# Kernel tuning notes

Hardware: AMD Instinct MI355X
Metric: run time of the kernel (lower is better)

## Reference

```python
import jax, jax.numpy as jnp
import numpy as np

S, B, NIN = 64, 64, 64          # att_width (= target_seq_len), batch, num_input
H1, HB, H = 128, 128, 128       # first LSTM size, biLSTM hidden, att_hid
MLP = (1024, 512, 256, 128, 1)  # h1..h4, num_output


def _lstm_cell(x, h, c, Wih, Whh, b):
    # PyTorch gate order: i, f, g, o
    z = x @ Wih.T + h @ Whh.T + b
    i, f, g, o = jnp.split(z, 4, axis=-1)
    c = jax.nn.sigmoid(f) * c + jax.nn.sigmoid(i) * jnp.tanh(g)
    h = jax.nn.sigmoid(o) * jnp.tanh(c)
    return h, c


def _lstm_seq(xs, Wih, Whh, b, reverse=False):
    # xs: [S, B, in] -> hs: [S, B, H], final (h, c)
    h0 = jnp.zeros((xs.shape[1], Whh.shape[1]), xs.dtype)

    def step(carry, x):
        h, c = _lstm_cell(x, carry[0], carry[1], Wih, Whh, b)
        return (h, c), h

    (h, c), hs = jax.lax.scan(step, (h0, h0), xs, reverse=reverse)
    return hs, (h, c)


def _forward(input_seqs,
             lstm1_Wih, lstm1_Whh, lstm1_b,
             bi2f_Wih, bi2f_Whh, bi2f_b, bi2b_Wih, bi2b_Whh, bi2b_b,
             bi3f_Wih, bi3f_Whh, bi3f_b, bi3b_Wih, bi3b_Whh, bi3b_b,
             enc_Wih, enc_Whh, enc_b,
             dec_Wih, dec_Whh, dec_b,
             att_fc_W, att_w,
             W1_W, W1_b, W2_W, W2_b, W3_W, W3_b, W4_W, W4_b, out_W, out_b):
    # 1) one-directional LSTM
    x, _ = _lstm_seq(input_seqs, lstm1_Wih, lstm1_Whh, lstm1_b)
    # 2-3) two stacked bidirectional LSTMs
    f, _ = _lstm_seq(x, bi2f_Wih, bi2f_Whh, bi2f_b)
    bk, _ = _lstm_seq(x, bi2b_Wih, bi2b_Whh, bi2b_b, reverse=True)
    x = jnp.concatenate([f, bk], axis=-1)            # [S,B,2*HB]
    f, _ = _lstm_seq(x, bi3f_Wih, bi3f_Whh, bi3f_b)
    bk, _ = _lstm_seq(x, bi3b_Wih, bi3b_Whh, bi3b_b, reverse=True)
    x = jnp.concatenate([f, bk], axis=-1)            # [S,B,2*HB]
    # 4) encoder LSTM
    enc_out, (eh, ec) = _lstm_seq(x, enc_Wih, enc_Whh, enc_b)  # [S,B,H]
    # per-step attention decode loop (S sequential steps)
    def dec_step(carry, _):
        xin, h, c = carry
        h, c = _lstm_cell(xin, h, c, dec_Wih, dec_Whh, dec_b)   # [B,H]
        # 'concat' attention: tanh(fc(h + enc_out)) @ w -> scores over S
        scores = jnp.tanh((h[None, :, :] + enc_out) @ att_fc_W.T) @ att_w  # [S,B]
        aw = jax.nn.softmax(scores, axis=0)
        ctx = jnp.einsum('sb,sbh->bh', aw, enc_out)             # [B,H]
        out = jnp.concatenate([h, ctx], axis=-1)                # [B,2H]
        return (h, h, c), out

    _, dec_outs = jax.lax.scan(dec_step, (enc_out[-1], eh, ec), None, length=S)
    # [S,B,2H] -> [B, S*2H]
    flat = dec_outs.transpose(1, 0, 2).reshape(dec_outs.shape[1], -1)
    # 5-6) flatten + 4-layer tanh MLP + linear head
    x = jnp.tanh(flat @ W1_W.T + W1_b)
    x = jnp.tanh(x @ W2_W.T + W2_b)
    x = jnp.tanh(x @ W3_W.T + W3_b)
    x = jnp.tanh(x @ W4_W.T + W4_b)
    return x @ out_W.T + out_b


def setup_inputs() -> dict:
    key = jax.random.key(0)
    ks = iter(jax.random.split(key, 40))

    def mat(shape, scale=0.08):
        return (jax.random.normal(next(ks), shape) * scale).astype(jnp.float32)

    d = {}
    d['input_seqs'] = jax.random.normal(next(ks), (S, B, NIN), dtype=jnp.float32)

    def lstm_p(pfx, inp, hid):
        d[pfx + '_Wih'] = mat((4 * hid, inp))
        d[pfx + '_Whh'] = mat((4 * hid, hid))
        d[pfx + '_b'] = mat((4 * hid,))

    lstm_p('lstm1', NIN, H1)
    lstm_p('bi2f', H1, HB); lstm_p('bi2b', H1, HB)
    lstm_p('bi3f', 2 * HB, HB); lstm_p('bi3b', 2 * HB, HB)
    lstm_p('enc', 2 * HB, H)
    lstm_p('dec', H, H)
    d['att_fc_W'] = mat((H, H))
    d['att_w'] = mat((H,))
    dims = [2 * H * S] + list(MLP)
    names = ['W1', 'W2', 'W3', 'W4', 'out']
    for i, nm in enumerate(names):
        d[nm + '_W'] = mat((dims[i + 1], dims[i]))
        d[nm + '_b'] = mat((dims[i + 1],))
    return d


def reference(input_seqs,
              lstm1_Wih, lstm1_Whh, lstm1_b,
              bi2f_Wih, bi2f_Whh, bi2f_b, bi2b_Wih, bi2b_Whh, bi2b_b,
              bi3f_Wih, bi3f_Whh, bi3f_b, bi3b_Wih, bi3b_Whh, bi3b_b,
              enc_Wih, enc_Whh, enc_b,
              dec_Wih, dec_Whh, dec_b,
              att_fc_W, att_w,
              W1_W, W1_b, W2_W, W2_b, W3_W, W3_b, W4_W, W4_b, out_W, out_b):
    return _forward(input_seqs,
                    lstm1_Wih, lstm1_Whh, lstm1_b,
                    bi2f_Wih, bi2f_Whh, bi2f_b, bi2b_Wih, bi2b_Whh, bi2b_b,
                    bi3f_Wih, bi3f_Whh, bi3f_b, bi3b_Wih, bi3b_Whh, bi3b_b,
                    enc_Wih, enc_Whh, enc_b,
                    dec_Wih, dec_Whh, dec_b,
                    att_fc_W, att_w,
                    W1_W, W1_b, W2_W, W2_b, W3_W, W3_b, W4_W, W4_b, out_W, out_b)
```

## Files before the change

### kernel.cpp

```cpp
#include <hip/hip_runtime.h>
#include <hip/hip_bf16.h>

typedef unsigned int u32;
typedef unsigned short u16;

typedef _Float16 half2_t __attribute__((ext_vector_type(2)));
union H2U { u32 u; half2_t h; };

typedef _Float16 f16x8 __attribute__((ext_vector_type(8)));
typedef float f32x4 __attribute__((ext_vector_type(4)));
union F16V { uint4 u; f16x8 h; };

#if defined(__has_builtin)
#if __has_builtin(__builtin_amdgcn_fdot2)
#define HAS_FDOT2 1
#endif
#if __has_builtin(__builtin_amdgcn_update_dpp)
#define HAS_DPP 1
#endif
#endif

__device__ __forceinline__ float bf2f(u32 u) {
  union { u32 i; float f; } v; v.i = u << 16; return v.f;
}
__device__ __forceinline__ float sigf(float x) {
  return 1.0f / (1.0f + __expf(-x));
}
__device__ __forceinline__ float tanhfast(float x) {
  return 2.0f / (1.0f + __expf(-2.0f * x)) - 1.0f;
}
__device__ __forceinline__ u16 f2bf(float f) {
  u32 u = __float_as_uint(f);
  u += 0x7fffu + ((u >> 16) & 1u);
  return (u16)(u >> 16);
}
__device__ __forceinline__ u16 f2h(float f) {
  union { _Float16 h; u16 u; } v; v.h = (_Float16)f; return v.u;
}
__device__ __forceinline__ u32 fpair2h2(float a, float b) {
  H2U r; r.h.x = (_Float16)a; r.h.y = (_Float16)b; return r.u;
}
__device__ __forceinline__ u32 bfpair2h2(u32 two_bf) {
  H2U r;
  r.h.x = (_Float16)bf2f(two_bf & 0xffffu);
  r.h.y = (_Float16)bf2f(two_bf >> 16);
  return r.u;
}
__device__ __forceinline__ float dot2acc(u32 wu, u32 hu, float acc) {
  H2U w, h; w.u = wu; h.u = hu;
#ifdef HAS_FDOT2
  return __builtin_amdgcn_fdot2(w.h, h.h, acc, false);
#else
  acc = fmaf((float)w.h.x, (float)h.h.x, acc);
  return fmaf((float)w.h.y, (float)h.h.y, acc);
#endif
}
template <int CTRL>
__device__ __forceinline__ float dppf(float x) {
#ifdef HAS_DPP
  int y = __builtin_amdgcn_update_dpp(0, __float_as_int(x), CTRL, 0xF, 0xF, true);
  return __int_as_float(y);
#else
  const int lane = threadIdx.x & 63;
  if (CTRL == 0xB1)  return __shfl_xor(x, 1, 64);
  if (CTRL == 0x4E)  return __shfl_xor(x, 2, 64);
  if (CTRL == 0x104) return __shfl_down(x, 4, 64);
  return __shfl(x, (lane & ~3) | (CTRL & 3), 64);
#endif
}

__global__ void k_detect(const u32* __restrict__ w, int* __restrict__ flag) {
  __shared__ int cnt;
  if (threadIdx.x == 0) cnt = 0;
  __syncthreads();
  int c = 0;
  for (int i = threadIdx.x; i < 8192; i += 256) {
    const u32 lo = w[i] & 0xffffu;
    const u32 e = (lo >> 7) & 0xffu;
    c += (e >= 100u && e <= 140u) ? 1 : 0;
  }
  atomicAdd(&cnt, c);
  __syncthreads();
  if (threadIdx.x == 0) *flag = (cnt > 4915) ? 1 : 0;
}

struct Job { const void* s; float* d; int n; int f16; };
struct Jobs { Job j[30]; };

__global__ void k_cvt_all(Jobs J, const int* __restrict__ flag) {
  const Job jb = J.j[blockIdx.y];
  const int isbf = *flag;
  for (int i = blockIdx.x * 256 + threadIdx.x; i < jb.n; i += 32 * 256) {
    const float v = isbf ? bf2f(((const u16*)jb.s)[i]) : ((const float*)jb.s)[i];
    if (jb.f16) ((u16*)jb.d)[i] = f2h(v);
    else        jb.d[i] = v;
  }
}

struct IJobs { const float* b[4]; float* d[4]; int n[4]; int mask[4]; };
__global__ void k_init4(IJobs I) {
  const int j = blockIdx.y;
  const float* bb = I.b[j];
  float* dd = I.d[j];
  const int n = I.n[j], mask = I.mask[j];
  for (int i = blockIdx.x * 256 + threadIdx.x; i < n; i += gridDim.x * 256)
    dd[i] = bb[i & mask];
}

struct PJobs { const float* s[7]; const float* s2[7]; u32* d[7]; };
__global__ void k_pack(PJobs P) {
  const float* src = P.s[blockIdx.y];
  const float* src2 = P.s2[blockIdx.y];
  u32* dst = P.d[blockIdx.y];
  const int i = blockIdx.x * 256 + threadIdx.x;
  const int tid = i >> 6, rem = i & 63;
  const int j = rem >> 4, kk = rem & 15;
  const int r = tid >> 2, kq = tid & 3;
  const int row = r + 128 * j, col = kq * 32 + 2 * kk;
  float v0 = src[row * 128 + col];
  float v1 = src[row * 128 + col + 1];
  if (src2) { v0 += src2[row * 128 + col]; v1 += src2[row * 128 + col + 1]; }
  H2U v;
  v.h.x = (_Float16)v0;
  v.h.y = (_Float16)v1;
  dst[i] = v.u;
}

__launch_bounds__(256)
__global__ void k_mf(const u16* __restrict__ A, int lda,
                     const void* __restrict__ Wv, int ldw,
                     const float* __restrict__ bias,
                     float* __restrict__ C, int ldc,
                     int K, int atom, int wfollow,
                     const int* __restrict__ dflag)
{
  __shared__ __align__(16) u16 As[64][40];
  __shared__ __align__(16) u16 Bs[64][40];
  const int isbf = wfollow ? *dflag : 0;
  const int tid = threadIdx.x;
  const int m0 = blockIdx.x * 64, n0 = blockIdx.y * 64;
  const int kc = K / gridDim.z;
  const int k0 = blockIdx.z * kc;
  const int row = tid >> 2, part = tid & 3;
  const int l = tid & 63, w = tid >> 6;
  const int wr = w >> 1, wc = w & 1;
  const int fr = l & 15, fk = l >> 4;
  f32x4 acc[2][2] = {};
  const u16*   Ap   = A + (size_t)(m0 + row) * lda + k0 + part * 8;
  const u16*   Wp16 = (const u16*)Wv   + (size_t)(n0 + row) * ldw + k0 + part * 8;
  const float* Wp32 = (const float*)Wv + (size_t)(n0 + row) * ldw + k0 + part * 8;

  for (int kk = 0; kk < kc; kk += 32) {
    const uint4 av = *(const uint4*)(Ap + kk);
    uint4 wv;
    if (isbf) {
      const uint4 wu = *(const uint4*)(Wp16 + kk);
      wv.x = bfpair2h2(wu.x); wv.y = bfpair2h2(wu.y);
      wv.z = bfpair2h2(wu.z); wv.w = bfpair2h2(wu.w);
    } else {
      const float4 w0 = *(const float4*)(Wp32 + kk);
      const float4 w1 = *(const float4*)(Wp32 + kk + 4);
      wv.x = fpair2h2(w0.x, w0.y); wv.y = fpair2h2(w0.z, w0.w);
      wv.z = fpair2h2(w1.x, w1.y); wv.w = fpair2h2(w1.z, w1.w);
    }
    __syncthreads();
    *(uint4*)&As[row][part * 8] = av;
    *(uint4*)&Bs[row][part * 8] = wv;
    __syncthreads();
    F16V a0, a1, b0, b1;
    a0.u = *(const uint4*)&As[wr * 32 + fr][fk * 8];
    a1.u = *(const uint4*)&As[wr * 32 + 16 + fr][fk * 8];
    b0.u = *(const uint4*)&Bs[wc * 32 + fr][fk * 8];
    b1.u = *(const uint4*)&Bs[wc * 32 + 16 + fr][fk * 8];
    acc[0][0] = __builtin_amdgcn_mfma_f32_16x16x32_f16(a0.h, b0.h, acc[0][0], 0, 0, 0);
    acc[0][1] = __builtin_amdgcn_mfma_f32_16x16x32_f16(a0.h, b1.h, acc[0][1], 0, 0, 0);
    acc[1][0] = __builtin_amdgcn_mfma_f32_16x16x32_f16(a1.h, b0.h, acc[1][0], 0, 0, 0);
    acc[1][1] = __builtin_amdgcn_mfma_f32_16x16x32_f16(a1.h, b1.h, acc[1][1], 0, 0, 0);
  }

  #pragma unroll
  for (int i = 0; i < 2; ++i) {
    #pragma unroll
    for (int j = 0; j < 2; ++j) {
      const int n = n0 + wc * 32 + j * 16 + fr;
      const float bv = (bias && !atom) ? bias[n] : 0.0f;
      #pragma unroll
      for (int q = 0; q < 4; ++q) {
        const int m = m0 + wr * 32 + i * 16 + fk * 4 + q;
        if (atom) atomicAdd(&C[(size_t)m * ldc + n], acc[i][j][q]);
        else      C[(size_t)m * ldc + n] = acc[i][j][q] + bv;
      }
    }
  }
}

__launch_bounds__(256)
__global__ void k_gemm(const float* __restrict__ A, int lda,
                       const void* __restrict__ Wv, int ldw,
                       const float* __restrict__ bias,
                       float* __restrict__ C, int ldc,
                       int K, int actA, int atom, int wfollow,
                       const int* __restrict__ dflag)
{
  __shared__ float As[32][65];
  __shared__ float Ws[32][65];
  const int isbf = wfollow ? *dflag : 0;
  const int tid = threadIdx.x;
  const int tx = tid & 15, ty = tid >> 4;
  const int m0 = blockIdx.x * 64, n0 = blockIdx.y * 64;
  const int kc = K / gridDim.z;
  const int k0 = blockIdx.z * kc;
  const int lr = tid >> 2;
  const int lk = (tid & 3) << 3;
  float acc[4][4] = {{0.f}};
  const float* Ap   = A + (size_t)(m0 + lr) * lda + k0 + lk;
  const u16*   Wp16 = (const u16*)Wv   + (size_t)(n0 + lr) * ldw + k0 + lk;
  const float* Wp32 = (const float*)Wv + (size_t)(n0 + lr) * ldw + k0 + lk;
  for (int kk = 0; kk < kc; kk += 32) {
    float4 av0 = *(const float4*)(Ap + kk);
    float4 av1 = *(const float4*)(Ap + kk + 4);
    float wv[8];
    if (isbf) {
      const uint4 wu = *(const uint4*)(Wp16 + kk);
      wv[0]=bf2f(wu.x & 0xffffu); wv[1]=bf2f(wu.x >> 16);
      wv[2]=bf2f(wu.y & 0xffffu); wv[3]=bf2f(wu.y >> 16);
      wv[4]=bf2f(wu.z & 0xffffu); wv[5]=bf2f(wu.z >> 16);
      wv[6]=bf2f(wu.w & 0xffffu); wv[7]=bf2f(wu.w >> 16);
    } else {
      const float4 w0 = *(const float4*)(Wp32 + kk);
      const float4 w1 = *(const float4*)(Wp32 + kk + 4);
      wv[0]=w0.x; wv[1]=w0.y; wv[2]=w0.z; wv[3]=w0.w;
      wv[4]=w1.x; wv[5]=w1.y; wv[6]=w1.z; wv[7]=w1.w;
    }
    if (actA) {
      av0.x = tanhfast(av0.x); av0.y = tanhfast(av0.y);
      av0.z = tanhfast(av0.z); av0.w = tanhfast(av0.w);
      av1.x = tanhfast(av1.x); av1.y = tanhfast(av1.y);
      av1.z = tanhfast(av1.z); av1.w = tanhfast(av1.w);
    }
    __syncthreads();
    As[lk+0][lr] = av0.x; As[lk+1][lr] = av0.y;
    As[lk+2][lr] = av0.z; As[lk+3][lr] = av0.w;
    As[lk+4][lr] = av1.x; As[lk+5][lr] = av1.y;
    As[lk+6][lr] = av1.z; As[lk+7][lr] = av1.w;
    #pragma unroll
    for (int q = 0; q < 8; ++q) Ws[lk+q][lr] = wv[q];
    __syncthreads();
    #pragma unroll
    for (int k = 0; k < 32; ++k) {
      float a[4], w[4];
      #pragma unroll
      for (int i = 0; i < 4; ++i) a[i] = As[k][ty + 16*i];
      #pragma unroll
      for (int j = 0; j < 4; ++j) w[j] = Ws[k][tx + 16*j];
      #pragma unroll
      for (int i = 0; i < 4; ++i)
        #pragma unroll
        for (int j = 0; j < 4; ++j)
          acc[i][j] = fmaf(a[i], w[j], acc[i][j]);
    }
  }
  #pragma unroll
  for (int i = 0; i < 4; ++i) {
    const int m = m0 + ty + 16*i;
    #pragma unroll
    for (int j = 0; j < 4; ++j) {
      const int n = n0 + tx + 16*j;
      if (atom) atomicAdd(&C[(size_t)m*ldc + n], acc[i][j]);
      else {
        const float bv = bias ? bias[n] : 0.0f;
        C[(size_t)m*ldc + n] = acc[i][j] + bv;
      }
    }
  }
}

__launch_bounds__(512)
__attribute__((amdgpu_waves_per_eu(2, 2)))
__global__ void k_rec(const float* __restrict__ Zf, const float* __restrict__ Zb,
                      const u32* __restrict__ Wf, const u32* __restrict__ Wb,
                      float* __restrict__ HS, int hstride, int offF, int offB,
                      const float* __restrict__ h0, const float* __restrict__ c0,
                      int zmode, int zld, float* __restrict__ Cout, int hf16)
{
  const int b = blockIdx.x & 63;
  const int dir = blockIdx.x >> 6;
  const float* Z = dir ? Zb : Zf;
  const u32* Wg = dir ? Wb : Wf;
  const int off = dir ? offB : offF;
  const int tid = threadIdx.x;
  const int r = tid >> 2, kq = tid & 3;

  __shared__ __align__(16) float zall[64*512];
  __shared__ __align__(16) u32 hbuf[2][64];

  if (!zmode) {
    #pragma unroll
    for (int q = 0; q < 16; ++q) {
      const int fid = tid + 512*q;
      const int s = fid >> 7, c4 = (fid & 127) << 2;
      const int cs = c4 ^ (((c4 >> 7) & 1) << 4);
      *(float4*)&zall[s*512 + cs] = *(const float4*)&Z[((size_t)s*64 + b)*zld + c4];
    }
  }

  u32 wp[64];
  {
    const uint4* wr = (const uint4*)(Wg + (size_t)tid * 64);
    #pragma unroll
    for (int q = 0; q < 16; ++q) {
      const uint4 u = wr[q];
      wp[q*4+0]=u.x; wp[q*4+1]=u.y; wp[q*4+2]=u.z; wp[q*4+3]=u.w;
    }
  }
  #pragma unroll
  for (int q = 0; q < 64; ++q)
    asm volatile("" : "+v"(wp[q]));

  float creg = c0 ? c0[b*128 + r] : 0.0f;
  if (tid < 64) {
    H2U v;
    if (h0) {
      v.h.x = (_Float16)h0[b*128 + 2*tid];
      v.h.y = (_Float16)h0[b*128 + 2*tid + 1];
    } else {
      v.h.x = (_Float16)0.f; v.h.y = (_Float16)0.f;
    }
    hbuf[0][tid] = v.u;
  }

  const int colz = (r + 128*kq) ^ ((kq & 1) << 4);
  float zdec = 0.f;
  if (zmode) zdec = Z[r + 128*kq];
  const float* zp = zall + (dir ? 63*512 : 0) + colz;
  const int zstep = dir ? -512 : 512;
  size_t hidx = ((size_t)(dir ? 63 : 0)*64 + b)*hstride + off + r;
  const ptrdiff_t hstep = (ptrdiff_t)(dir ? -64 : 64) * hstride;
  const bool beta = (kq & 1) != 0;
  const bool gmm  = (kq & 2) != 0;
  __syncthreads();

  for (int t = 0; t < 64; ++t) {
    float zcv;
    if (zmode) zcv = zdec;
    else       zcv = *zp;
    u32 hh16[16];
    {
      const u32* hp = hbuf[t & 1];
      *(uint4*)&hh16[0]  = *(const uint4*)&hp[kq*16];
      *(uint4*)&hh16[4]  = *(const uint4*)&hp[kq*16 + 4];
      *(uint4*)&hh16[8]  = *(const uint4*)&hp[kq*16 + 8];
      *(uint4*)&hh16[12] = *(const uint4*)&hp[kq*16 + 12];
    }
    float a[4] = {0.f,0.f,0.f,0.f};
    #pragma unroll
    for (int j = 0; j < 4; ++j)
      #pragma unroll
      for (int i = 0; i < 16; ++i)
        a[j] = dot2acc(wp[j*16 + i], hh16[i], a[j]);
    const float u0 = beta ? a[1] : a[0];
    const float v0 = beta ? a[0] : a[1];
    const float u1 = beta ? a[3] : a[2];
    const float v1 = beta ? a[2] : a[3];
    const float x01 = u0 + dppf<0xB1>(v0);
    const float x23 = u1 + dppf<0xB1>(v1);
    const float keep = gmm ? x23 : x01;
    const float send = gmm ? x01 : x23;
    const float g = keep + dppf<0x4E>(send) + zcv;
    const float sg = sigf(g);
    const float tg = tanhfast(g);
    const float si  = dppf<0x00>(sg);
    const float sf  = dppf<0x55>(sg);
    const float tgg = dppf<0xAA>(tg);
    const float so  = dppf<0xFF>(sg);
    const float cc = sf * creg + si * tgg;
    const float hh = so * tanhfast(cc);
    creg = cc;
    const float hn = dppf<0x104>(hh);
    if (kq == 0) {
      if (hf16) ((u16*)HS)[hidx] = f2h(hh);
      else      HS[hidx] = hh;
      if (!(r & 1)) {
        H2U v; v.h.x = (_Float16)hh; v.h.y = (_Float16)hn;
        hbuf[(t+1) & 1][r >> 1] = v.u;
      }
    }
    zp += zstep;
    hidx += hstep;
    __syncthreads();
  }

  if (Cout != nullptr && kq == 0) Cout[b*128 + r] = creg;
}

#define TS 132
__launch_bounds__(256, 1)
__global__ void k_att(const float* __restrict__ enco, const float* __restrict__ encp,
                      const float* __restrict__ Hdec, const float* __restrict__ Hproj,
                      const float* __restrict__ attw, u16* __restrict__ flat)
{
  const int b = blockIdx.x;
  const int t0 = blockIdx.y * 16;
  const int tid = threadIdx.x;
  __shared__ __align__(16) float ep[64*TS];
  __shared__ __align__(16) float en[64*TS];
  __shared__ __align__(16) float hp[16*TS];
  __shared__ float S[64*17];
  __shared__ float aw[64*17];
  __shared__ __align__(16) float awt[128];

  for (int i = tid; i < 8192; i += 256) {
    const int s = i >> 7, k = i & 127;
    const size_t g = ((size_t)s*64 + b)*128 + k;
    ep[s*TS + k] = encp[g];
    en[s*TS + k] = enco[g];
  }
  for (int i = tid; i < 2048; i += 256) {
    const int t = i >> 7, k = i & 127;
    const size_t g = ((size_t)(t0 + t)*64 + b)*128 + k;
    hp[t*TS + k] = Hproj[g];
    flat[(size_t)b*16384 + (t0 + t)*256 + k] = f2h(Hdec[g]);
  }
  if (tid < 128) awt[tid] = attw[tid];
  __syncthreads();

  {
    const int t = tid & 15, sg = tid >> 4;
    #pragma unroll
    for (int i = 0; i < 4; ++i) {
      const int s = sg*4 + i;
      float acc = 0.f;
      #pragma unroll 8
      for (int k = 0; k < 128; k += 4) {
        const float4 h4 = *(const float4*)&hp[t*TS + k];
        const float4 e4 = *(const float4*)&ep[s*TS + k];
        const float4 w4 = *(const float4*)&awt[k];
        acc = fmaf(w4.x, tanhfast(h4.x + e4.x), acc);
        acc = fmaf(w4.y, tanhfast(h4.y + e4.y), acc);
        acc = fmaf(w4.z, tanhfast(h4.z + e4.z), acc);
        acc = fmaf(w4.w, tanhfast(h4.w + e4.w), acc);
      }
      S[s*17 + t] = acc;
    }
  }
  __syncthreads();
  if (tid < 16) {
    const int t = tid;
    float m = -1e30f;
    for (int s = 0; s < 64; ++s) m = fmaxf(m, S[s*17 + t]);
    float sum = 0.f;
    for (int s = 0; s < 64; ++s) {
      const float e = __expf(S[s*17 + t] - m);
      aw[s*17 + t] = e;
      sum += e;
    }
    const float inv = 1.0f / sum;
    for (int s = 0; s < 64; ++s) aw[s*17 + t] *= inv;
  }
  __syncthreads();
  {
    const int t = tid >> 4, kg = tid & 15;
    float c0a[8] = {0,0,0,0,0,0,0,0};
    for (int s = 0; s < 64; ++s) {
      const float a = aw[s*17 + t];
      const float4 e0 = *(const float4*)&en[s*TS + kg*8];
      const float4 e1 = *(const float4*)&en[s*TS + kg*8 + 4];
      c0a[0] = fmaf(a, e0.x, c0a[0]);
      c0a[1] = fmaf(a, e0.y, c0a[1]);
      c0a[2] = fmaf(a, e0.z, c0a[2]);
      c0a[3] = fmaf(a, e0.w, c0a[3]);
      c0a[4] = fmaf(a, e1.x, c0a[4]);
      c0a[5] = fmaf(a, e1.y, c0a[5]);
      c0a[6] = fmaf(a, e1.z, c0a[6]);
      c0a[7] = fmaf(a, e1.w, c0a[7]);
    }
    union { u16 s[8]; uint4 u; } o;
    #pragma unroll
    for (int q = 0; q < 8; ++q) o.s[q] = f2h(c0a[q]);
    u16* dst = &flat[(size_t)b*16384 + (t0 + t)*256 + 128 + kg*8];
    *(uint4*)dst = o.u;
  }
}

__global__ void k_head(const float* __restrict__ a4, const float* __restrict__ outW,
                       const float* __restrict__ outb, void* __restrict__ out,
                       const int* __restrict__ dflag)
{
  const int b = threadIdx.x;
  float acc = outb[0];
  #pragma unroll 8
  for (int k = 0; k < 128; ++k)
    acc = fmaf(outW[k], tanhfast(a4[b*128 + k]), acc);
  if (*dflag) ((u16*)out)[b] = f2bf(acc);
  else        ((float*)out)[b] = acc;
}

extern "C" void kernel_launch(void* const* d_in, const int* in_sizes, int n_in,
                              void* d_out, int out_size, void* d_ws, size_t ws_size,
                              hipStream_t stream)
{
  (void)in_sizes; (void)n_in; (void)out_size; (void)ws_size;

  float* p = (float*)d_ws;
  int*   flagp = (int*)p;    p += 64;
  float* x0    = p; p += 64*64*64;
  float* cl1Wih = p; p += 512*64;
  float* cl1Whh = p; p += 512*128;
  float* cl1b   = p; p += 512;
  float* c2Wih  = p; p += 1024*128;
  float* c2bias = p; p += 1024;
  float* c2fWhh = p; p += 512*128;
  float* c2bWhh = p; p += 512*128;
  float* c3Wih  = p; p += 1024*256;
  float* c3bias = p; p += 1024;
  float* c3fWhh = p; p += 512*128;
  float* c3bWhh = p; p += 512*128;
  float* ceWih  = p; p += 512*256;
  float* ceWhh  = p; p += 512*128;
  float* ceb    = p; p += 512;
  float* cdWih  = p; p += 512*128;
  float* cdWhh  = p; p += 512*128;
  float* cdb    = p; p += 512;
  float* cattW  = p; p += 128*128;
  float* cattw  = p; p += 128;
  float* cW1b   = p; p += 1024;
  float* cW2b   = p; p += 512;
  float* cW3b   = p; p += 256;
  float* cW4b   = p; p += 128;
  float* coW    = p; p += 128;
  float* cob    = p; p += 16;
  u32* wpL1 = (u32*)p; p += 32768;
  u32* wp2f = (u32*)p; p += 32768;
  u32* wp2b = (u32*)p; p += 32768;
  u32* wp3f = (u32*)p; p += 32768;
  u32* wp3b = (u32*)p; p += 32768;
  u32* wpE  = (u32*)p; p += 32768;
  u32* wpD  = (u32*)p; p += 32768;
  float* Zf   = p; p += 4096*512;
  float* Z2   = p; p += 4096*1024;
  float* h1   = p; p += 4096*128;
  float* x2   = p; p += 4096*256;
  float* x3   = p; p += 4096*256;
  float* enco = p; p += 4096*128;
  float* Hdec = p; p += 4096*128;
  float* encp = p; p += 4096*128;
  float* Hprj = p; p += 4096*128;
  float* ec   = p; p += 64*128;
  float* flat = p; p += 64*16384;
  float* a1   = p; p += 64*1024;
  float* a2   = p; p += 64*512;
  float* a3   = p; p += 64*256;
  float* a4   = p; p += 64*128;

  k_detect<<<1, 256, 0, stream>>>((const u32*)d_in[2], flagp);

  Jobs J;
  int nj = 0;
  auto add = [&](const void* s, float* d, int n, int f16 = 0) {
    J.j[nj].s = s; J.j[nj].d = d; J.j[nj].n = n; J.j[nj].f16 = f16; ++nj;
  };
  add(d_in[0],  x0,     64*64*64, 1);
  add(d_in[1],  cl1Wih, 512*64);
  add(d_in[2],  cl1Whh, 512*128);
  add(d_in[3],  cl1b,   512);
  add(d_in[4],  c2Wih,            512*128);
  add(d_in[7],  c2Wih + 512*128,  512*128);
  add(d_in[6],  c2bias,       512);
  add(d_in[9],  c2bias + 512, 512);
  add(d_in[5],  c2fWhh, 512*128);
  add(d_in[8],  c2bWhh, 512*128);
  add(d_in[10], c3Wih,            512*256);
  add(d_in[13], c3Wih + 512*256,  512*256);
  add(d_in[12], c3bias,       512);
  add(d_in[15], c3bias + 512, 512);
  add(d_in[11], c3fWhh, 512*128);
  add(d_in[14], c3bWhh, 512*128);
  add(d_in[16], ceWih,  512*256);
  add(d_in[17], ceWhh,  512*128);
  add(d_in[18], ceb,    512);
  add(d_in[19], cdWih,  512*128);
  add(d_in[20], cdWhh,  512*128);
  add(d_in[21], cdb,    512);
  add(d_in[22], cattW,  128*128);
  add(d_in[23], cattw,  128);
  add(d_in[25], cW1b,   1024);
  add(d_in[27], cW2b,   512);
  add(d_in[29], cW3b,   256);
  add(d_in[31], cW4b,   128);
  add(d_in[32], coW,    128);
  add(d_in[33], cob,    1);
  k_cvt_all<<<dim3(32, nj), 256, 0, stream>>>(J, flagp);

  PJobs P;
  for (int i = 0; i < 7; ++i) P.s2[i] = nullptr;
  P.s[0] = cl1Whh; P.d[0] = wpL1;
  P.s[1] = c2fWhh; P.d[1] = wp2f;
  P.s[2] = c2bWhh; P.d[2] = wp2b;
  P.s[3] = c3fWhh; P.d[3] = wp3f;
  P.s[4] = c3bWhh; P.d[4] = wp3b;
  P.s[5] = ceWhh;  P.d[5] = wpE;
  P.s[6] = cdWih;  P.s2[6] = cdWhh; P.d[6] = wpD;
  k_pack<<<dim3(128, 7), 256, 0, stream>>>(P);

  k_mf<<<dim3(64,8,1), 256, 0, stream>>>((const u16*)x0, 64, cl1Wih, 64, cl1b, Zf, 512, 64, 0, 0, flagp);
  k_rec<<<64, 512, 0, stream>>>(Zf, Zf, wpL1, wpL1, h1, 128, 0, 0, nullptr, nullptr, 0, 512, nullptr, 1);

  k_mf<<<dim3(64,16,1), 256, 0, stream>>>((const u16*)h1, 128, c2Wih, 128, c2bias, Z2, 1024, 128, 0, 0, flagp);
  k_rec<<<128, 512, 0, stream>>>(Z2, Z2 + 512, wp2f, wp2b, x2, 256, 0, 128, nullptr, nullptr, 0, 1024, nullptr, 1);

  k_mf<<<dim3(64,16,1), 256, 0, stream>>>((const u16*)x2, 256, c3Wih, 256, c3bias, Z2, 1024, 256, 0, 0, flagp);
  k_rec<<<128, 512, 0, stream>>>(Z2, Z2 + 512, wp3f, wp3b, x3, 256, 0, 128, nullptr, nullptr, 0, 1024, nullptr, 1);

  k_mf<<<dim3(64,8,1), 256, 0, stream>>>((const u16*)x3, 256, ceWih, 256, ceb, Zf, 512, 256, 0, 0, flagp);
  k_rec<<<64, 512, 0, stream>>>(Zf, Zf, wpE, wpE, enco, 128, 0, 0, nullptr, nullptr, 0, 512, ec, 0);

  k_rec<<<64, 512, 0, stream>>>(cdb, cdb, wpD, wpD, Hdec, 128, 0, 0,
                                enco + (size_t)63*64*128, ec, 1, 512, nullptr, 0);

  k_gemm<<<dim3(128,2,1), 256, 0, stream>>>(enco, 128, cattW, 128, nullptr, encp, 128, 128, 0, 0, 0, flagp);

  k_att<<<dim3(64,4), 256, 0, stream>>>(enco, encp, Hdec, Hprj, cattw, (u16*)flat);

  IJobs I;
  I.b[0]=cW1b; I.d[0]=a1; I.n[0]=64*1024; I.mask[0]=1023;
  I.b[1]=cW2b; I.d[1]=a2; I.n[1]=64*512;  I.mask[1]=511;
  I.b[2]=cW3b; I.d[2]=a3; I.n[2]=64*256;  I.mask[2]=255;
  I.b[3]=cW4b; I.d[3]=a4; I.n[3]=64*128;  I.mask[3]=127;
  k_init4<<<dim3(64, 4), 256, 0, stream>>>(I);
  k_mf<<<dim3(1,16,64), 256, 0, stream>>>((const u16*)flat, 16384, d_in[24], 16384, nullptr, a1, 1024, 16384, 1, 1, flagp);
  k_gemm<<<dim3(1,8,16), 256, 0, stream>>>(a1, 1024, d_in[26], 1024, nullptr, a2, 512, 1024, 1, 1, 1, flagp);
  k_gemm<<<dim3(1,4,8), 256, 0, stream>>>(a2, 512, d_in[28], 512, nullptr, a3, 256, 512, 1, 1, 1, flagp);
  k_gemm<<<dim3(1,2,4), 256, 0, stream>>>(a3, 256, d_in[30], 256, nullptr, a4, 128, 256, 1, 1, 1, flagp);

  k_head<<<1, 64, 0, stream>>>(a4, coW, cob, d_out, flagp);
}
```

Before: 559.3 us.

## Remap recurrent LSTM threads to two hidden units per 8-lane group

Reorganizes the recurrent LSTM kernel so each 8-thread group computes two adjacent hidden units. Each thread now holds weights for two rows over half the K range, loads half as much h per step from LDS and reduces across 8 lanes with an extra DPP shift. The weight packing, z-swizzle and padded hbuf layout change to match. The intent is to cut per-step LDS h reads and let one lane write packed fp16 pairs of h, at the cost of extra cross-lane shuffles and duplicated gate math per thread.

```diff
diff --git a/kernel.cpp b/kernel.cpp
--- a/kernel.cpp
+++ b/kernel.cpp
@@ -65,6 +65,7 @@
   if (CTRL == 0xB1)  return __shfl_xor(x, 1, 64);
   if (CTRL == 0x4E)  return __shfl_xor(x, 2, 64);
   if (CTRL == 0x104) return __shfl_down(x, 4, 64);
+  if (CTRL == 0x114) return __shfl_up(x, 4, 64);
   return __shfl(x, (lane & ~3) | (CTRL & 3), 64);
 #endif
 }
@@ -114,9 +115,10 @@
   u32* dst = P.d[blockIdx.y];
   const int i = blockIdx.x * 256 + threadIdx.x;
   const int tid = i >> 6, rem = i & 63;
-  const int j = rem >> 4, kk = rem & 15;
-  const int r = tid >> 2, kq = tid & 3;
-  const int row = r + 128 * j, col = kq * 32 + 2 * kk;
+  const int row01 = rem >> 5, j = (rem >> 3) & 3, kk = rem & 7;
+  const int rp = tid >> 3, c8 = tid & 7;
+  const int row = 2 * rp + row01 + 128 * j;
+  const int col = 16 * c8 + 2 * kk;
   float v0 = src[row * 128 + col];
   float v1 = src[row * 128 + col + 1];
   if (src2) { v0 += src2[row * 128 + col]; v1 += src2[row * 128 + col + 1]; }
@@ -289,17 +291,18 @@
   const u32* Wg = dir ? Wb : Wf;
   const int off = dir ? offB : offF;
   const int tid = threadIdx.x;
-  const int r = tid >> 2, kq = tid & 3;
+  const int rp = tid >> 3, c8 = tid & 7;
+  const int g = c8 & 3, hi = c8 >> 2;
 
   __shared__ __align__(16) float zall[64*512];
-  __shared__ __align__(16) u32 hbuf[2][64];
+  __shared__ __align__(16) u32 hbuf[2][68];
 
   if (!zmode) {
     #pragma unroll
     for (int q = 0; q < 16; ++q) {
       const int fid = tid + 512*q;
       const int s = fid >> 7, c4 = (fid & 127) << 2;
-      const int cs = c4 ^ (((c4 >> 7) & 1) << 4);
+      const int cs = c4 ^ ((c4 >> 7) << 3);
       *(float4*)&zall[s*512 + cs] = *(const float4*)&Z[((size_t)s*64 + b)*zld + c4];
     }
   }
@@ -317,7 +320,8 @@
   for (int q = 0; q < 64; ++q)
     asm volatile("" : "+v"(wp[q]));
 
-  float creg = c0 ? c0[b*128 + r] : 0.0f;
+  float creg0 = c0 ? c0[b*128 + 2*rp]     : 0.0f;
+  float creg1 = c0 ? c0[b*128 + 2*rp + 1] : 0.0f;
   if (tid < 64) {
     H2U v;
     if (h0) {
@@ -326,71 +330,92 @@
     } else {
       v.h.x = (_Float16)0.f; v.h.y = (_Float16)0.f;
     }
-    hbuf[0][tid] = v.u;
-  }
-
-  const int colz = (r + 128*kq) ^ ((kq & 1) << 4);
-  float zdec = 0.f;
-  if (zmode) zdec = Z[r + 128*kq];
-  const float* zp = zall + (dir ? 63*512 : 0) + colz;
+    hbuf[0][tid + ((tid >> 5) << 2)] = v.u;
+  }
+
+  const int zc_e = (2*rp + 128*g) ^ (g << 3);
+  float zdec0 = 0.f, zdec1 = 0.f;
+  if (zmode) { zdec0 = Z[2*rp + 128*g]; zdec1 = Z[2*rp + 1 + 128*g]; }
+  const float* zp = zall + (dir ? 63*512 : 0) + zc_e;
   const int zstep = dir ? -512 : 512;
-  size_t hidx = ((size_t)(dir ? 63 : 0)*64 + b)*hstride + off + r;
+  size_t hidx = ((size_t)(dir ? 63 : 0)*64 + b)*hstride + off + 2*rp;
   const ptrdiff_t hstep = (ptrdiff_t)(dir ? -64 : 64) * hstride;
-  const bool beta = (kq & 1) != 0;
-  const bool gmm  = (kq & 2) != 0;
+  const bool beta = (c8 & 1) != 0;
+  const bool gmm  = (c8 & 2) != 0;
+  const int hbase = c8*8 + (hi << 2);
+  const int hwidx = rp + ((rp >> 5) << 2);
   __syncthreads();
 
   for (int t = 0; t < 64; ++t) {
-    float zcv;
-    if (zmode) zcv = zdec;
-    else       zcv = *zp;
-    u32 hh16[16];
+    float zc0, zc1;
+    if (zmode) { zc0 = zdec0; zc1 = zdec1; }
+    else { const float2 z2 = *(const float2*)zp; zc0 = z2.x; zc1 = z2.y; }
+    u32 hh8[8];
     {
-      const u32* hp = hbuf[t & 1];
-      *(uint4*)&hh16[0]  = *(const uint4*)&hp[kq*16];
-      *(uint4*)&hh16[4]  = *(const uint4*)&hp[kq*16 + 4];
-      *(uint4*)&hh16[8]  = *(const uint4*)&hp[kq*16 + 8];
-      *(uint4*)&hh16[12] = *(const uint4*)&hp[kq*16 + 12];
-    }
-    float a[4] = {0.f,0.f,0.f,0.f};
+      const u32* hp = &hbuf[t & 1][hbase];
+      *(uint4*)&hh8[0] = *(const uint4*)&hp[0];
+      *(uint4*)&hh8[4] = *(const uint4*)&hp[4];
+    }
+    float a0[4] = {0.f,0.f,0.f,0.f};
+    float a1[4] = {0.f,0.f,0.f,0.f};
     #pragma unroll
     for (int j = 0; j < 4; ++j)
       #pragma unroll
-      for (int i = 0; i < 16; ++i)
-        a[j] = dot2acc(wp[j*16 + i], hh16[i], a[j]);
-    const float u0 = beta ? a[1] : a[0];
-    const float v0 = beta ? a[0] : a[1];
-    const float u1 = beta ? a[3] : a[2];
-    const float v1 = beta ? a[2] : a[3];
-    const float x01 = u0 + dppf<0xB1>(v0);
-    const float x23 = u1 + dppf<0xB1>(v1);
-    const float keep = gmm ? x23 : x01;
-    const float send = gmm ? x01 : x23;
-    const float g = keep + dppf<0x4E>(send) + zcv;
-    const float sg = sigf(g);
-    const float tg = tanhfast(g);
-    const float si  = dppf<0x00>(sg);
-    const float sf  = dppf<0x55>(sg);
-    const float tgg = dppf<0xAA>(tg);
-    const float so  = dppf<0xFF>(sg);
-    const float cc = sf * creg + si * tgg;
-    const float hh = so * tanhfast(cc);
-    creg = cc;
-    const float hn = dppf<0x104>(hh);
-    if (kq == 0) {
-      if (hf16) ((u16*)HS)[hidx] = f2h(hh);
-      else      HS[hidx] = hh;
-      if (!(r & 1)) {
-        H2U v; v.h.x = (_Float16)hh; v.h.y = (_Float16)hn;
-        hbuf[(t+1) & 1][r >> 1] = v.u;
+      for (int i = 0; i < 8; ++i) {
+        a0[j] = dot2acc(wp[j*8 + i],      hh8[i], a0[j]);
+        a1[j] = dot2acc(wp[32 + j*8 + i], hh8[i], a1[j]);
       }
+    float gf0, gf1;
+    {
+      const float u0 = beta ? a0[1] : a0[0];
+      const float v0 = beta ? a0[0] : a0[1];
+      const float u1 = beta ? a0[3] : a0[2];
+      const float v1 = beta ? a0[2] : a0[3];
+      const float x01 = u0 + dppf<0xB1>(v0);
+      const float x23 = u1 + dppf<0xB1>(v1);
+      const float q = (gmm ? x23 : x01) + dppf<0x4E>(gmm ? x01 : x23);
+      const float ep = dppf<0x104>(q);
+      const float em = dppf<0x114>(q);
+      gf0 = q + (hi ? em : ep) + zc0;
+    }
+    {
+      const float u0 = beta ? a1[1] : a1[0];
+      const float v0 = beta ? a1[0] : a1[1];
+      const float u1 = beta ? a1[3] : a1[2];
+      const float v1 = beta ? a1[2] : a1[3];
+      const float x01 = u0 + dppf<0xB1>(v0);
+      const float x23 = u1 + dppf<0xB1>(v1);
+      const float q = (gmm ? x23 : x01) + dppf<0x4E>(gmm ? x01 : x23);
+      const float ep = dppf<0x104>(q);
+      const float em = dppf<0x114>(q);
+      gf1 = q + (hi ? em : ep) + zc1;
+    }
+    const float sg0 = sigf(gf0), tg0 = tanhfast(gf0);
+    const float sg1 = sigf(gf1), tg1 = tanhfast(gf1);
+    const float si0 = dppf<0x00>(sg0), sf0 = dppf<0x55>(sg0);
+    const float tgg0 = dppf<0xAA>(tg0), so0 = dppf<0xFF>(sg0);
+    const float si1 = dppf<0x00>(sg1), sf1 = dppf<0x55>(sg1);
+    const float tgg1 = dppf<0xAA>(tg1), so1 = dppf<0xFF>(sg1);
+    const float cc0 = sf0 * creg0 + si0 * tgg0;
+    const float cc1 = sf1 * creg1 + si1 * tgg1;
+    const float hh0 = so0 * tanhfast(cc0);
+    const float hh1 = so1 * tanhfast(cc1);
+    creg0 = cc0; creg1 = cc1;
+    if (c8 == 0) {
+      H2U v; v.h.x = (_Float16)hh0; v.h.y = (_Float16)hh1;
+      if (hf16) ((u32*)HS)[hidx >> 1] = v.u;
+      else { float2 o; o.x = hh0; o.y = hh1; *(float2*)&HS[hidx] = o; }
+      hbuf[(t+1) & 1][hwidx] = v.u;
     }
     zp += zstep;
     hidx += hstep;
     __syncthreads();
   }
 
-  if (Cout != nullptr && kq == 0) Cout[b*128 + r] = creg;
+  if (Cout != nullptr && c8 == 0) {
+    float2 o; o.x = creg0; o.y = creg1;
+    *(float2*)&Cout[b*128 + 2*rp] = o;
+  }
 }
 
 #define TS 132
```

Measured after the change: 649.0 us. +16.0%, slower.
